# Kernel optimization log

Hardware: AMD Instinct MI355X
Metric: run time of the kernel (lower is better)

## Reference

```python
import jax, jax.numpy as jnp
import numpy as np

DIM = 128
HEADS = 4
DIM_HEAD = 32
EPS = 1e-5


def layer_norm(x, w, b):
    mu = jnp.mean(x, axis=-1, keepdims=True)
    var = jnp.mean(jnp.square(x - mu), axis=-1, keepdims=True)
    return (x - mu) * jax.lax.rsqrt(var + EPS) * w + b


def setup_inputs() -> dict:
    key = jax.random.key(0)
    ks = jax.random.split(key, 16)
    B, N, D, bH, bW = 2, 6, DIM, 50, 50
    iH, iW = 24, 56
    HD = HEADS * DIM_HEAD
    w = lambda k, shp: (jax.random.normal(k, shp, jnp.float32) * 0.02)
    inp = {
        "q": jax.random.normal(ks[0], (B, N, D, bH, bW), jnp.float32),
        "k": jax.random.normal(ks[1], (B, N, D, iH, iW), jnp.float32),
        "v": jax.random.normal(ks[2], (B, N, D, iH, iW), jnp.float32),
        "skip": jax.random.normal(ks[3], (B, D, bH, bW), jnp.float32),
        "ln_q_w": jnp.ones((D,), jnp.float32), "ln_q_b": jnp.zeros((D,), jnp.float32),
        "wq": w(ks[4], (D, HD)), "bq": jnp.zeros((HD,), jnp.float32),
        "ln_k_w": jnp.ones((D,), jnp.float32), "ln_k_b": jnp.zeros((D,), jnp.float32),
        "wk": w(ks[5], (D, HD)), "bk": jnp.zeros((HD,), jnp.float32),
        "ln_v_w": jnp.ones((D,), jnp.float32), "ln_v_b": jnp.zeros((D,), jnp.float32),
        "wv": w(ks[6], (D, HD)), "bv": jnp.zeros((HD,), jnp.float32),
        "wo": w(ks[7], (HD, D)), "bo": jnp.zeros((D,), jnp.float32),
        "ln_pre_w": jnp.ones((D,), jnp.float32), "ln_pre_b": jnp.zeros((D,), jnp.float32),
        "w1": w(ks[8], (D, 2 * D)), "b1": jnp.zeros((2 * D,), jnp.float32),
        "w2": w(ks[9], (2 * D, D)), "b2": jnp.zeros((D,), jnp.float32),
        "ln_post_w": jnp.ones((D,), jnp.float32), "ln_post_b": jnp.zeros((D,), jnp.float32),
    }
    return inp


def reference(q, k, v, skip,
              ln_q_w, ln_q_b, wq, bq,
              ln_k_w, ln_k_b, wk, bk,
              ln_v_w, ln_v_b, wv, bv,
              wo, bo, ln_pre_w, ln_pre_b,
              w1, b1, w2, b2, ln_post_w, ln_post_b):
    B, N, D, bH, bW = q.shape
    iH, iW = k.shape[-2:]
    Q, K = bH * bW, iH * iW
    scale = D ** (-0.5)  # NOTE: original uses dim**-0.5, not dim_head

    # queries: (B,N,D,Q) -> (B,N,Q,D) -> LN -> linear -> (B,N,Q,H,Dh)
    qf = jnp.transpose(q.reshape(B, N, D, Q), (0, 1, 3, 2))
    qh = (layer_norm(qf, ln_q_w, ln_q_b) @ wq + bq).reshape(B, N, Q, HEADS, DIM_HEAD)
    # keys: (B,N,D,K) -> (B,N,K,D)
    kf = jnp.transpose(k.reshape(B, N, D, K), (0, 1, 3, 2))
    kh = (layer_norm(kf, ln_k_w, ln_k_b) @ wk + bk).reshape(B, N, K, HEADS, DIM_HEAD)
    # values: (B,N,D,iH,iW) -> (B,N,iH,iW,D) -> (B,N*K,D)
    vf = jnp.transpose(v, (0, 1, 3, 4, 2)).reshape(B, N * K, D)
    vh = (layer_norm(vf, ln_v_w, ln_v_b) @ wv + bv).reshape(B, N * K, HEADS, DIM_HEAD)

    # logits: (B,N,Q,K,H) -> (B,Q,N*K,H), softmax over combined N*K axis
    logits = scale * jnp.einsum('bnqmd,bnkmd->bnqkm', qh, kh)
    logits = jnp.transpose(logits, (0, 2, 1, 3, 4)).reshape(B, Q, N * K, HEADS)
    att = jax.nn.softmax(logits, axis=-2)

    a = jnp.einsum('bqkm,bkmd->bqmd', att, vh).reshape(B, Q, HEADS * DIM_HEAD)
    z = a @ wo + bo  # (B,Q,D)
    z = z + jnp.transpose(skip.reshape(B, D, Q), (0, 2, 1))
    z = layer_norm(z, ln_pre_w, ln_pre_b)
    z = z + (jax.nn.gelu(z @ w1 + b1, approximate=False) @ w2 + b2)
    z = layer_norm(z, ln_post_w, ln_post_b)
    return jnp.transpose(z.reshape(B, bH, bW, D), (0, 3, 1, 2))
```

## Files before the change

kernel.cpp:

```cpp
#include <hip/hip_runtime.h>
#include <hip/hip_bf16.h>

#define QP 2500
#define KP 1344
#define SCALE 0.088388347648318447f
#define LOG2E 1.4426950408889634f
#define LNEPS 1e-5f

typedef __attribute__((ext_vector_type(8))) short bf16x8;
typedef __attribute__((ext_vector_type(4))) float f32x4;

__device__ inline ushort f2bf(float x) {
  uint u = __float_as_uint(x);
  return (ushort)((u + 0x7fffu + ((u >> 16) & 1u)) >> 16);
}

union Frag8 { uint2 u[2]; bf16x8 f; ushort us[8]; };

__device__ inline bf16x8 ldfrag_swz(const char* rowbase, int colbyte, int C) {
  Frag8 t;
  t.u[0] = *(const uint2*)(rowbase + ((colbyte) ^ C));
  t.u[1] = *(const uint2*)(rowbase + ((colbyte + 8) ^ C));
  return t.f;
}

__device__ inline uint pk2(float a, float b) {
  union { __hip_bfloat162 h; uint u; } cv;
  cv.h = __float22bfloat162_rn(make_float2(a, b));
  return cv.u;
}

__device__ inline void gld16(const ushort* g, ushort* l) {
  __builtin_amdgcn_global_load_lds(
      (const __attribute__((address_space(1))) void*)g,
      (__attribute__((address_space(3))) void*)l, 16, 0, 0);
}

__global__ __launch_bounds__(256) void wprep_kernel(
    const float* __restrict__ wq, const float* __restrict__ wk, const float* __restrict__ wv,
    ushort* __restrict__ wtq, ushort* __restrict__ wtk, ushort* __restrict__ wtv)
{
  const float* W = (blockIdx.y == 0) ? wq : (blockIdx.y == 1) ? wk : wv;
  ushort* WT = (blockIdx.y == 0) ? wtq : (blockIdx.y == 1) ? wtk : wtv;
  const int t = threadIdx.x;
  const int idx = blockIdx.x * 1024 + t * 4;
  const int k = idx >> 7, j0 = idx & 127;
  float4 rd = *(const float4*)&W[idx];
  WT[(j0 + 0) * 128 + k] = f2bf(rd.x);
  WT[(j0 + 1) * 128 + k] = f2bf(rd.y);
  WT[(j0 + 2) * 128 + k] = f2bf(rd.z);
  WT[(j0 + 3) * 128 + k] = f2bf(rd.w);
}

__global__ __launch_bounds__(256) void wprep2_kernel(
    const float* __restrict__ wo, const float* __restrict__ w1, const float* __restrict__ w2,
    ushort* __restrict__ woT, ushort* __restrict__ w1T, ushort* __restrict__ w2T)
{
  const int y = blockIdx.y;
  const float* W; ushort* WT; int jsh, K, total;
  if (y == 0)      { W = wo; WT = woT; jsh = 7; K = 128; total = 16384; }
  else if (y == 1) { W = w1; WT = w1T; jsh = 8; K = 128; total = 32768; }
  else             { W = w2; WT = w2T; jsh = 7; K = 256; total = 32768; }
  const int idx = blockIdx.x * 1024 + threadIdx.x * 4;
  if (idx >= total) return;
  const int k = idx >> jsh, j0 = idx & ((1 << jsh) - 1);
  float4 rd = *(const float4*)&W[idx];
  WT[(j0 + 0) * K + k] = f2bf(rd.x);
  WT[(j0 + 1) * K + k] = f2bf(rd.y);
  WT[(j0 + 2) * K + k] = f2bf(rd.z);
  WT[(j0 + 3) * K + k] = f2bf(rd.w);
}

__global__ __launch_bounds__(256) void proj_kernel(
    const float* __restrict__ qin, const float* __restrict__ kin, const float* __restrict__ vin,
    const float* __restrict__ lnqw, const float* __restrict__ lnqb,
    const float* __restrict__ lnkw, const float* __restrict__ lnkb,
    const float* __restrict__ lnvw, const float* __restrict__ lnvb,
    const ushort* __restrict__ wtq_, const ushort* __restrict__ wtk_, const ushort* __restrict__ wtv_,
    const float* __restrict__ bq_, const float* __restrict__ bk_, const float* __restrict__ bv_,
    ushort* __restrict__ qout, ushort* __restrict__ kout, ushort* __restrict__ vtout)
{
  const int z = blockIdx.z;
  if (z > 0 && blockIdx.x >= 21) return;

  const float *in, *lnw, *lnb, *bias;
  const ushort* WT;
  int P;
  if (z == 0)      { in = qin; lnw = lnqw; lnb = lnqb; WT = wtq_; bias = bq_; P = QP; }
  else if (z == 1) { in = kin; lnw = lnkw; lnb = lnkb; WT = wtk_; bias = bk_; P = KP; }
  else             { in = vin; lnw = lnvw; lnb = lnvb; WT = wtv_; bias = bv_; P = KP; }

  __shared__ __align__(16) ushort xb[64][128];
  __shared__ __align__(16) ushort wt[128][128];
  __shared__ float ps[4][64], pq[4][64];
  __shared__ float mu_s[64], rs_s[64];

  const int bn = blockIdx.y;
  const int p0 = blockIdx.x * 64;
  const int t  = threadIdx.x;
  const int w = t >> 6, lane = t & 63, g = lane >> 4, ln15 = lane & 15;

  #pragma unroll
  for (int i = 0; i < 8; ++i) {
    int idx8 = t + 256 * i;
    int j = idx8 >> 4, ck = (idx8 & 15) * 16;
    *(uint4*)((char*)wt + j * 256 + (ck ^ ((j & 7) << 4))) =
        *(const uint4*)((const char*)WT + j * 256 + ck);
  }

  const float* src = in + ((size_t)bn * 128) * P + p0;
  const int p = t & 63, dq = t >> 6;
  float xv[32];
  float s = 0.f, s2 = 0.f;
  #pragma unroll
  for (int kk = 0; kk < 32; ++kk) {
    int d = dq + 4 * kk;
    float v = (p0 + p < P) ? src[(size_t)d * P + p] : 0.f;
    xv[kk] = v; s += v; s2 += v * v;
  }
  ps[dq][p] = s; pq[dq][p] = s2;
  __syncthreads();
  if (t < 64) {
    float a = ps[0][t] + ps[1][t] + ps[2][t] + ps[3][t];
    float b = pq[0][t] + pq[1][t] + pq[2][t] + pq[3][t];
    float mu = a * (1.f / 128.f);
    float var = b * (1.f / 128.f) - mu * mu;
    mu_s[t] = mu; rs_s[t] = rsqrtf(var + LNEPS);
  }
  __syncthreads();
  {
    const float mu = mu_s[p], rs = rs_s[p];
    const int CW = (p & 7) << 4;
    #pragma unroll
    for (int kk = 0; kk < 32; ++kk) {
      int d = dq + 4 * kk;
      float v = (xv[kk] - mu) * rs * lnw[d] + lnb[d];
      *(ushort*)((char*)xb + p * 256 + ((2 * d) ^ CW)) = f2bf(v);
    }
  }
  __syncthreads();

  const int prow = w * 16 + ln15;
  const char* xrow = (const char*)xb + prow * 256;
  const int CX = (prow & 7) << 4;
  const int CB = (ln15 & 7) << 4;
  const f32x4 zf = {0.f, 0.f, 0.f, 0.f};
  f32x4 acc[8];
  #pragma unroll
  for (int jc = 0; jc < 8; ++jc) acc[jc] = zf;

  #pragma unroll
  for (int ks = 0; ks < 4; ++ks) {
    bf16x8 a = ldfrag_swz(xrow, ks * 64 + g * 16, CX);
    #pragma unroll
    for (int jc = 0; jc < 8; ++jc) {
      bf16x8 b = ldfrag_swz((const char*)wt + (jc * 16 + ln15) * 256, ks * 64 + g * 16, CB);
      acc[jc] = __builtin_amdgcn_mfma_f32_16x16x32_bf16(a, b, acc[jc], 0, 0, 0);
    }
  }

  if (z == 0) {
    const float os = SCALE * LOG2E;
    #pragma unroll
    for (int jc = 0; jc < 8; ++jc) {
      const float bj = bias[jc * 16 + ln15];
      #pragma unroll
      for (int r = 0; r < 4; ++r) {
        int pr = p0 + w * 16 + 4 * g + r;
        if (pr < P)
          qout[((size_t)bn * P + pr) * 128 + jc * 16 + ln15] = f2bf((acc[jc][r] + bj) * os);
      }
    }
  } else if (z == 1) {
    #pragma unroll
    for (int jc = 0; jc < 8; ++jc) {
      const int j = jc * 16 + ln15;
      const int h = j >> 5, dh = j & 31, gk = dh >> 3, pos = dh & 7;
      const float bj = bias[j];
      #pragma unroll
      for (int r4 = 0; r4 < 4; ++r4) {
        int pp = p0 + w * 16 + 4 * g + r4;
        int kt = pp >> 6, r = pp & 63;
        int ch = (gk + (r >> 1)) & 3;
        kout[(size_t)((bn * 4 + h) * 21 + kt) * 2048 + r * 32 + ch * 8 + pos] =
            f2bf(acc[jc][r4] + bj);
      }
    }
  } else {
    #pragma unroll
    for (int jc = 0; jc < 8; ++jc) {
      const int j = jc * 16 + ln15;
      const int h = j >> 5, rdh = j & 31;
      const float bj = bias[j];
      #pragma unroll
      for (int r4 = 0; r4 < 4; ++r4) {
        int pp = p0 + w * 16 + 4 * g + r4;
        int kt = pp >> 6, kk = pp & 63;
        int ch = (kk >> 3) ^ (rdh & 7);
        vtout[(size_t)((bn * 4 + h) * 21 + kt) * 2048 + rdh * 64 + ch * 8 + (kk & 7)] =
            f2bf(acc[jc][r4] + bj);
      }
    }
  }
}

__global__ __launch_bounds__(256, 4) void attn_kernel(
    const ushort* __restrict__ qh, const ushort* __restrict__ kimg,
    const ushort* __restrict__ vimg, float* __restrict__ aw,
    float* __restrict__ ml)
{
  __shared__ __align__(16) ushort Kb[2][2048];
  __shared__ __align__(16) ushort Vb[2][2048];
  __shared__ __align__(16) ushort Ps[4][32][64];

  const int lin = blockIdx.x + 20 * (blockIdx.y + 4 * blockIdx.z);
  const int sid = (lin & 7) * 120 + (lin >> 3);
  const int bx = sid % 20;
  const int hh = (sid / 20) & 3;
  const int bn = sid / 80;

  const int q0 = bx * 128;
  const int t = threadIdx.x;
  const int w = t >> 6, lane = t & 63;
  const int g = lane >> 4, ln15 = lane & 15;
  const int C = ((ln15 & 7) << 4) | (((ln15 >> 3) & 1) << 3);
  const int kch = (g + (ln15 >> 1)) & 3;
  const int vch0 = (0 + g) ^ (ln15 & 7);
  const int vch1 = (4 + g) ^ (ln15 & 7);

  bf16x8 qf0, qf1;
  {
    Frag8 z_; z_.u[0] = make_uint2(0, 0); z_.u[1] = make_uint2(0, 0);
    int qr0 = q0 + w * 32 + ln15;
    int qr1 = qr0 + 16;
    qf0 = (qr0 < QP) ? *(const bf16x8*)&qh[((size_t)bn * QP + qr0) * 128 + hh * 32 + g * 8] : z_.f;
    qf1 = (qr1 < QP) ? *(const bf16x8*)&qh[((size_t)bn * QP + qr1) * 128 + hh * 32 + g * 8] : z_.f;
  }

  Frag8 onesU;
  #pragma unroll
  for (int i = 0; i < 8; ++i) onesU.us[i] = 0x3F80;
  const bf16x8 ones = onesU.f;

  const ushort* ksrc = kimg + (size_t)((bn * 4 + hh) * 21) * 2048 + w * 512 + lane * 8;
  const ushort* vsrc = vimg + (size_t)((bn * 4 + hh) * 21) * 2048 + w * 512 + lane * 8;

  gld16(ksrc, &Kb[0][w * 512]);
  gld16(vsrc, &Vb[0][w * 512]);
  __syncthreads();

  const f32x4 zf = {0.f, 0.f, 0.f, 0.f};
  f32x4 o00 = zf, o01 = zf, o10 = zf, o11 = zf, ol0 = zf, ol1 = zf;

  for (int kt = 0; kt < 21; ++kt) {
    const int cur = kt & 1;
    if (kt < 20) {
      gld16(ksrc + (size_t)(kt + 1) * 2048, &Kb[cur ^ 1][w * 512]);
      gld16(vsrc + (size_t)(kt + 1) * 2048, &Vb[cur ^ 1][w * 512]);
    }

    const char* Kbase = (const char*)Kb[cur];
    const char* Vbase = (const char*)Vb[cur];
    char* Pw = (char*)Ps[w];

    f32x4 s0[4], s1[4];
    #pragma unroll
    for (int kb = 0; kb < 4; ++kb) {
      bf16x8 kf = *(const bf16x8*)(Kbase + (kb * 16 + ln15) * 64 + kch * 16);
      s0[kb] = __builtin_amdgcn_mfma_f32_16x16x32_bf16(kf, qf0, zf, 0, 0, 0);
      s1[kb] = __builtin_amdgcn_mfma_f32_16x16x32_bf16(kf, qf1, zf, 0, 0, 0);
    }

    {
      char* pr0 = Pw + ln15 * 128;
      char* pr1 = Pw + (16 + ln15) * 128;
      #pragma unroll
      for (int kb = 0; kb < 4; ++kb) {
        uint2 u;
        u.x = pk2(exp2f(s0[kb][0]), exp2f(s0[kb][1]));
        u.y = pk2(exp2f(s0[kb][2]), exp2f(s0[kb][3]));
        *(uint2*)(pr0 + ((kb * 32 + g * 8) ^ C)) = u;
        u.x = pk2(exp2f(s1[kb][0]), exp2f(s1[kb][1]));
        u.y = pk2(exp2f(s1[kb][2]), exp2f(s1[kb][3]));
        *(uint2*)(pr1 + ((kb * 32 + g * 8) ^ C)) = u;
      }
    }

    {
      const char* pr0 = Pw + ln15 * 128;
      const char* pr1 = Pw + (16 + ln15) * 128;
      #pragma unroll
      for (int kc = 0; kc < 2; ++kc) {
        bf16x8 pa0 = ldfrag_swz(pr0, kc * 64 + g * 16, C);
        bf16x8 pa1 = ldfrag_swz(pr1, kc * 64 + g * 16, C);
        const int vch = kc ? vch1 : vch0;
        bf16x8 vf0 = *(const bf16x8*)(Vbase + ln15 * 128 + vch * 16);
        bf16x8 vf1 = *(const bf16x8*)(Vbase + (16 + ln15) * 128 + vch * 16);
        o00 = __builtin_amdgcn_mfma_f32_16x16x32_bf16(pa0, vf0, o00, 0, 0, 0);
        o01 = __builtin_amdgcn_mfma_f32_16x16x32_bf16(pa0, vf1, o01, 0, 0, 0);
        o10 = __builtin_amdgcn_mfma_f32_16x16x32_bf16(pa1, vf0, o10, 0, 0, 0);
        o11 = __builtin_amdgcn_mfma_f32_16x16x32_bf16(pa1, vf1, o11, 0, 0, 0);
        ol0 = __builtin_amdgcn_mfma_f32_16x16x32_bf16(pa0, ones, ol0, 0, 0, 0);
        ol1 = __builtin_amdgcn_mfma_f32_16x16x32_bf16(pa1, ones, ol1, 0, 0, 0);
      }
    }
    __syncthreads();
  }

  if (ln15 == 0) {
    #pragma unroll
    for (int i = 0; i < 4; ++i) {
      int qr0 = q0 + w * 32 + 4 * g + i;
      int qr1 = qr0 + 16;
      if (qr0 < QP) ml[((size_t)bn * QP + qr0) * 4 + hh] = ol0[i];
      if (qr1 < QP) ml[((size_t)bn * QP + qr1) * 4 + hh] = ol1[i];
    }
  }
  #pragma unroll
  for (int i = 0; i < 4; ++i) {
    int qr0 = q0 + w * 32 + 4 * g + i;
    int qr1 = qr0 + 16;
    if (qr0 < QP) {
      size_t base = ((size_t)bn * QP + qr0) * 128 + hh * 32;
      aw[base + ln15] = o00[i];
      aw[base + 16 + ln15] = o01[i];
    }
    if (qr1 < QP) {
      size_t base = ((size_t)bn * QP + qr1) * 128 + hh * 32;
      aw[base + ln15] = o10[i];
      aw[base + 16 + ln15] = o11[i];
    }
  }
}

__global__ __launch_bounds__(256) void epilogue_kernel(
    const float* __restrict__ aw, const float* __restrict__ ml,
    const float* __restrict__ skip,
    const ushort* __restrict__ woT, const float* __restrict__ bo,
    const float* __restrict__ lnpw, const float* __restrict__ lnpb,
    const ushort* __restrict__ w1T, const float* __restrict__ b1,
    const ushort* __restrict__ w2T, const float* __restrict__ b2,
    const float* __restrict__ lnqw, const float* __restrict__ lnqb,
    float* __restrict__ out)
{
  __shared__ __align__(16) ushort xa[16][128];
  __shared__ __align__(16) ushort znb[16][128];
  __shared__ __align__(16) ushort hb[16][256];
  __shared__ float skp[128][17];
  __shared__ float2 red[4][16];
  __shared__ float mu_s[16], rs_s[16];
  __shared__ float cc[16][4];

  const int b = blockIdx.y;
  const int q0 = blockIdx.x * 16;
  const int t = threadIdx.x;
  const int w = t >> 6, lane = t & 63, g = lane >> 4, ln15 = lane & 15;
  const f32x4 zf = {0.f, 0.f, 0.f, 0.f};

  if (t < 64) {
    int r = t >> 2, h = t & 3;
    int qrow = q0 + r;
    float inv = 0.f;
    if (qrow < QP) {
      float sum = 0.f;
      #pragma unroll
      for (int n = 0; n < 6; ++n)
        sum += ml[((size_t)(b * 6 + n) * QP + qrow) * 4 + h];
      inv = 1.f / sum;
    }
    cc[r][h] = inv;
  }
  #pragma unroll
  for (int i = 0; i < 8; ++i) {
    int idx = t + 256 * i;
    int j = idx >> 4, r = idx & 15;
    int qrow = q0 + r;
    skp[j][r] = (qrow < QP) ? skip[((size_t)b * 128 + j) * QP + qrow] : 0.f;
  }
  __syncthreads();

  #pragma unroll
  for (int i = 0; i < 4; ++i) {
    int idx = t + 256 * i;
    int r = idx >> 6, jp = idx & 63;
    int qrow = q0 + r;
    float v0 = 0.f, v1 = 0.f;
    if (qrow < QP) {
      #pragma unroll
      for (int n = 0; n < 6; ++n) {
        float2 p = *(const float2*)&aw[((size_t)(b * 6 + n) * QP + qrow) * 128 + 2 * jp];
        v0 += p.x; v1 += p.y;
      }
      float iv = cc[r][jp >> 4];
      v0 *= iv; v1 *= iv;
    }
    *(uint*)((char*)xa + r * 256 + ((4 * jp) ^ ((r & 7) << 4))) = pk2(v0, v1);
  }
  __syncthreads();

  f32x4 acc1[2] = {zf, zf};
  #pragma unroll
  for (int ks = 0; ks < 4; ++ks) {
    bf16x8 a = ldfrag_swz((const char*)xa + ln15 * 256, ks * 64 + g * 16, (ln15 & 7) << 4);
    #pragma unroll
    for (int jc = 0; jc < 2; ++jc) {
      int j = (2 * w + jc) * 16 + ln15;
      bf16x8 bfr = *(const bf16x8*)&woT[j * 128 + ks * 32 + g * 8];
      acc1[jc] = __builtin_amdgcn_mfma_f32_16x16x32_bf16(a, bfr, acc1[jc], 0, 0, 0);
    }
  }
  float z[2][4];
  #pragma unroll
  for (int jc = 0; jc < 2; ++jc) {
    int j = (2 * w + jc) * 16 + ln15;
    float bj = bo[j];
    #pragma unroll
    for (int i = 0; i < 4; ++i)
      z[jc][i] = acc1[jc][i] + bj + skp[j][4 * g + i];
  }
  {
    float s_[4], q_[4];
    #pragma unroll
    for (int i = 0; i < 4; ++i) {
      s_[i] = z[0][i] + z[1][i];
      q_[i] = z[0][i] * z[0][i] + z[1][i] * z[1][i];
    }
    #pragma unroll
    for (int m = 1; m <= 8; m <<= 1) {
      #pragma unroll
      for (int i = 0; i < 4; ++i) {
        s_[i] += __shfl_xor(s_[i], m);
        q_[i] += __shfl_xor(q_[i], m);
      }
    }
    if (ln15 == 0) {
      #pragma unroll
      for (int i = 0; i < 4; ++i) red[w][4 * g + i] = make_float2(s_[i], q_[i]);
    }
  }
  __syncthreads();
  if (t < 16) {
    float S = red[0][t].x + red[1][t].x + red[2][t].x + red[3][t].x;
    float Q = red[0][t].y + red[1][t].y + red[2][t].y + red[3][t].y;
    float mu = S * (1.f / 128.f);
    float var = Q * (1.f / 128.f) - mu * mu;
    mu_s[t] = mu; rs_s[t] = rsqrtf(var + LNEPS);
  }
  __syncthreads();
  float zn[2][4];
  #pragma unroll
  for (int jc = 0; jc < 2; ++jc) {
    int j = (2 * w + jc) * 16 + ln15;
    float lw = lnpw[j], lb = lnpb[j];
    #pragma unroll
    for (int i = 0; i < 4; ++i) {
      int r = 4 * g + i;
      float v = (z[jc][i] - mu_s[r]) * rs_s[r] * lw + lb;
      zn[jc][i] = v;
      *(ushort*)((char*)znb + r * 256 + ((2 * j) ^ ((r & 7) << 4))) = f2bf(v);
    }
  }
  __syncthreads();

  f32x4 acc2[4] = {zf, zf, zf, zf};
  #pragma unroll
  for (int ks = 0; ks < 4; ++ks) {
    bf16x8 a = ldfrag_swz((const char*)znb + ln15 * 256, ks * 64 + g * 16, (ln15 & 7) << 4);
    #pragma unroll
    for (int jc2 = 0; jc2 < 4; ++jc2) {
      int j2 = (4 * w + jc2) * 16 + ln15;
      bf16x8 bfr = *(const bf16x8*)&w1T[j2 * 128 + ks * 32 + g * 8];
      acc2[jc2] = __builtin_amdgcn_mfma_f32_16x16x32_bf16(a, bfr, acc2[jc2], 0, 0, 0);
    }
  }
  #pragma unroll
  for (int jc2 = 0; jc2 < 4; ++jc2) {
    int j2 = (4 * w + jc2) * 16 + ln15;
    float bj = b1[j2];
    #pragma unroll
    for (int i = 0; i < 4; ++i) {
      float x = acc2[jc2][i] + bj;
      float ge = 0.5f * x * (1.f + erff(x * 0.70710678118654752f));
      int r = 4 * g + i;
      *(ushort*)((char*)hb + r * 512 + ((2 * j2) ^ ((r & 7) << 4))) = f2bf(ge);
    }
  }
  __syncthreads();

  f32x4 acc3[2] = {zf, zf};
  #pragma unroll
  for (int ks = 0; ks < 8; ++ks) {
    bf16x8 a = ldfrag_swz((const char*)hb + ln15 * 512, ks * 64 + g * 16, (ln15 & 7) << 4);
    #pragma unroll
    for (int jc = 0; jc < 2; ++jc) {
      int j = (2 * w + jc) * 16 + ln15;
      bf16x8 bfr = *(const bf16x8*)&w2T[j * 256 + ks * 32 + g * 8];
      acc3[jc] = __builtin_amdgcn_mfma_f32_16x16x32_bf16(a, bfr, acc3[jc], 0, 0, 0);
    }
  }
  float z2[2][4];
  #pragma unroll
  for (int jc = 0; jc < 2; ++jc) {
    int j = (2 * w + jc) * 16 + ln15;
    float bj = b2[j];
    #pragma unroll
    for (int i = 0; i < 4; ++i)
      z2[jc][i] = acc3[jc][i] + bj + zn[jc][i];
  }
  {
    float s_[4], q_[4];
    #pragma unroll
    for (int i = 0; i < 4; ++i) {
      s_[i] = z2[0][i] + z2[1][i];
      q_[i] = z2[0][i] * z2[0][i] + z2[1][i] * z2[1][i];
    }
    #pragma unroll
    for (int m = 1; m <= 8; m <<= 1) {
      #pragma unroll
      for (int i = 0; i < 4; ++i) {
        s_[i] += __shfl_xor(s_[i], m);
        q_[i] += __shfl_xor(q_[i], m);
      }
    }
    if (ln15 == 0) {
      #pragma unroll
      for (int i = 0; i < 4; ++i) red[w][4 * g + i] = make_float2(s_[i], q_[i]);
    }
  }
  __syncthreads();
  if (t < 16) {
    float S = red[0][t].x + red[1][t].x + red[2][t].x + red[3][t].x;
    float Q = red[0][t].y + red[1][t].y + red[2][t].y + red[3][t].y;
    float mu = S * (1.f / 128.f);
    float var = Q * (1.f / 128.f) - mu * mu;
    mu_s[t] = mu; rs_s[t] = rsqrtf(var + LNEPS);
  }
  __syncthreads();
  #pragma unroll
  for (int jc = 0; jc < 2; ++jc) {
    int j = (2 * w + jc) * 16 + ln15;
    float lw = lnqw[j], lb = lnqb[j];
    #pragma unroll
    for (int i = 0; i < 4; ++i) {
      int r = 4 * g + i;
      skp[j][r] = (z2[jc][i] - mu_s[r]) * rs_s[r] * lw + lb;
    }
  }
  __syncthreads();
  #pragma unroll
  for (int i = 0; i < 8; ++i) {
    int idx = t + 256 * i;
    int j = idx >> 4, r = idx & 15;
    int qrow = q0 + r;
    if (qrow < QP)
      out[((size_t)b * 128 + j) * QP + qrow] = skp[j][r];
  }
}

extern "C" void kernel_launch(void* const* d_in, const int* in_sizes, int n_in,
                              void* d_out, int out_size, void* d_ws, size_t ws_size,
                              hipStream_t stream) {
  const float* q       = (const float*)d_in[0];
  const float* k       = (const float*)d_in[1];
  const float* v       = (const float*)d_in[2];
  const float* skip    = (const float*)d_in[3];
  const float* ln_q_w  = (const float*)d_in[4];
  const float* ln_q_b  = (const float*)d_in[5];
  const float* wq      = (const float*)d_in[6];
  const float* bq      = (const float*)d_in[7];
  const float* ln_k_w  = (const float*)d_in[8];
  const float* ln_k_b  = (const float*)d_in[9];
  const float* wk      = (const float*)d_in[10];
  const float* bk      = (const float*)d_in[11];
  const float* ln_v_w  = (const float*)d_in[12];
  const float* ln_v_b  = (const float*)d_in[13];
  const float* wv      = (const float*)d_in[14];
  const float* bv      = (const float*)d_in[15];
  const float* wo      = (const float*)d_in[16];
  const float* bo      = (const float*)d_in[17];
  const float* ln_pre_w  = (const float*)d_in[18];
  const float* ln_pre_b  = (const float*)d_in[19];
  const float* w1      = (const float*)d_in[20];
  const float* b1      = (const float*)d_in[21];
  const float* w2      = (const float*)d_in[22];
  const float* b2      = (const float*)d_in[23];
  const float* ln_post_w = (const float*)d_in[24];
  const float* ln_post_b = (const float*)d_in[25];

  float* out = (float*)d_out;
  ushort* qhp  = (ushort*)d_ws;
  ushort* kimg = qhp + 3840000;
  ushort* vimg = kimg + 2064384;
  ushort* wtq  = vimg + 2064384;
  ushort* wtk  = wtq + 16384;
  ushort* wtv  = wtk + 16384;
  ushort* woT  = wtv + 16384;
  ushort* w1T  = woT + 16384;
  ushort* w2T  = w1T + 32768;
  float*  aw   = (float*)(w2T + 32768);
  float*  ml   = aw + 3840000;

  wprep_kernel<<<dim3(16, 3), 256, 0, stream>>>(wq, wk, wv, wtq, wtk, wtv);
  wprep2_kernel<<<dim3(32, 3), 256, 0, stream>>>(wo, w1, w2, woT, w1T, w2T);
  proj_kernel<<<dim3(40, 12, 3), 256, 0, stream>>>(q, k, v,
      ln_q_w, ln_q_b, ln_k_w, ln_k_b, ln_v_w, ln_v_b,
      wtq, wtk, wtv, bq, bk, bv, qhp, kimg, vimg);
  attn_kernel<<<dim3(20, 4, 12), 256, 0, stream>>>(qhp, kimg, vimg, aw, ml);
  epilogue_kernel<<<dim3(157, 2), 256, 0, stream>>>(aw, ml, skip, woT, bo,
      ln_pre_w, ln_pre_b, w1T, b1, w2T, b2, ln_post_w, ln_post_b, out);
}
```

Baseline: 112.4 us.

## Load K/V fragments directly from global in attention, merge weight-prep kernels

Result: faster. 109.7 us (-2.5%).

```diff
diff --git a/kernel.cpp b/kernel.cpp
--- a/kernel.cpp
+++ b/kernel.cpp
@@ -30,37 +30,22 @@
   return cv.u;
 }
 
-__device__ inline void gld16(const ushort* g, ushort* l) {
-  __builtin_amdgcn_global_load_lds(
-      (const __attribute__((address_space(1))) void*)g,
-      (__attribute__((address_space(3))) void*)l, 16, 0, 0);
-}
-
 __global__ __launch_bounds__(256) void wprep_kernel(
     const float* __restrict__ wq, const float* __restrict__ wk, const float* __restrict__ wv,
-    ushort* __restrict__ wtq, ushort* __restrict__ wtk, ushort* __restrict__ wtv)
-{
-  const float* W = (blockIdx.y == 0) ? wq : (blockIdx.y == 1) ? wk : wv;
-  ushort* WT = (blockIdx.y == 0) ? wtq : (blockIdx.y == 1) ? wtk : wtv;
-  const int t = threadIdx.x;
-  const int idx = blockIdx.x * 1024 + t * 4;
-  const int k = idx >> 7, j0 = idx & 127;
-  float4 rd = *(const float4*)&W[idx];
-  WT[(j0 + 0) * 128 + k] = f2bf(rd.x);
-  WT[(j0 + 1) * 128 + k] = f2bf(rd.y);
-  WT[(j0 + 2) * 128 + k] = f2bf(rd.z);
-  WT[(j0 + 3) * 128 + k] = f2bf(rd.w);
-}
-
-__global__ __launch_bounds__(256) void wprep2_kernel(
     const float* __restrict__ wo, const float* __restrict__ w1, const float* __restrict__ w2,
+    ushort* __restrict__ wtq, ushort* __restrict__ wtk, ushort* __restrict__ wtv,
     ushort* __restrict__ woT, ushort* __restrict__ w1T, ushort* __restrict__ w2T)
 {
   const int y = blockIdx.y;
   const float* W; ushort* WT; int jsh, K, total;
-  if (y == 0)      { W = wo; WT = woT; jsh = 7; K = 128; total = 16384; }
-  else if (y == 1) { W = w1; WT = w1T; jsh = 8; K = 128; total = 32768; }
-  else             { W = w2; WT = w2T; jsh = 7; K = 256; total = 32768; }
+  switch (y) {
+    case 0: W = wq; WT = wtq; jsh = 7; K = 128; total = 16384; break;
+    case 1: W = wk; WT = wtk; jsh = 7; K = 128; total = 16384; break;
+    case 2: W = wv; WT = wtv; jsh = 7; K = 128; total = 16384; break;
+    case 3: W = wo; WT = woT; jsh = 7; K = 128; total = 16384; break;
+    case 4: W = w1; WT = w1T; jsh = 8; K = 128; total = 32768; break;
+    default: W = w2; WT = w2T; jsh = 7; K = 256; total = 32768; break;
+  }
   const int idx = blockIdx.x * 1024 + threadIdx.x * 4;
   if (idx >= total) return;
   const int k = idx >> jsh, j0 = idx & ((1 << jsh) - 1);
@@ -209,8 +194,6 @@
     const ushort* __restrict__ vimg, float* __restrict__ aw,
     float* __restrict__ ml)
 {
-  __shared__ __align__(16) ushort Kb[2][2048];
-  __shared__ __align__(16) ushort Vb[2][2048];
   __shared__ __align__(16) ushort Ps[4][32][64];
 
   const int lin = blockIdx.x + 20 * (blockIdx.y + 4 * blockIdx.z);
@@ -242,34 +225,27 @@
   for (int i = 0; i < 8; ++i) onesU.us[i] = 0x3F80;
   const bf16x8 ones = onesU.f;
 
-  const ushort* ksrc = kimg + (size_t)((bn * 4 + hh) * 21) * 2048 + w * 512 + lane * 8;
-  const ushort* vsrc = vimg + (size_t)((bn * 4 + hh) * 21) * 2048 + w * 512 + lane * 8;
-
-  gld16(ksrc, &Kb[0][w * 512]);
-  gld16(vsrc, &Vb[0][w * 512]);
-  __syncthreads();
+  const size_t slab = (size_t)((bn * 4 + hh) * 21) * 2048;
+  const ushort* kfp = kimg + slab + ln15 * 32 + kch * 8;
+  const ushort* vb0 = vimg + slab + ln15 * 64;
+  const ushort* vb1 = vb0 + 16 * 64;
 
   const f32x4 zf = {0.f, 0.f, 0.f, 0.f};
   f32x4 o00 = zf, o01 = zf, o10 = zf, o11 = zf, ol0 = zf, ol1 = zf;
 
   for (int kt = 0; kt < 21; ++kt) {
-    const int cur = kt & 1;
-    if (kt < 20) {
-      gld16(ksrc + (size_t)(kt + 1) * 2048, &Kb[cur ^ 1][w * 512]);
-      gld16(vsrc + (size_t)(kt + 1) * 2048, &Vb[cur ^ 1][w * 512]);
-    }
-
-    const char* Kbase = (const char*)Kb[cur];
-    const char* Vbase = (const char*)Vb[cur];
+    const ushort* kp = kfp + (size_t)kt * 2048;
     char* Pw = (char*)Ps[w];
 
     f32x4 s0[4], s1[4];
+    __builtin_amdgcn_s_setprio(1);
     #pragma unroll
     for (int kb = 0; kb < 4; ++kb) {
-      bf16x8 kf = *(const bf16x8*)(Kbase + (kb * 16 + ln15) * 64 + kch * 16);
+      bf16x8 kf = *(const bf16x8*)(kp + kb * 512);
       s0[kb] = __builtin_amdgcn_mfma_f32_16x16x32_bf16(kf, qf0, zf, 0, 0, 0);
       s1[kb] = __builtin_amdgcn_mfma_f32_16x16x32_bf16(kf, qf1, zf, 0, 0, 0);
     }
+    __builtin_amdgcn_s_setprio(0);
 
     {
       char* pr0 = Pw + ln15 * 128;
@@ -287,24 +263,27 @@
     }
 
     {
-      const char* pr0 = Pw + ln15 * 128;
-      const char* pr1 = Pw + (16 + ln15) * 128;
+      const char* pr0 = (const char*)Ps[w] + ln15 * 128;
+      const char* pr1 = (const char*)Ps[w] + (16 + ln15) * 128;
+      const ushort* vt0 = vb0 + (size_t)kt * 2048;
+      const ushort* vt1 = vb1 + (size_t)kt * 2048;
       #pragma unroll
       for (int kc = 0; kc < 2; ++kc) {
         bf16x8 pa0 = ldfrag_swz(pr0, kc * 64 + g * 16, C);
         bf16x8 pa1 = ldfrag_swz(pr1, kc * 64 + g * 16, C);
         const int vch = kc ? vch1 : vch0;
-        bf16x8 vf0 = *(const bf16x8*)(Vbase + ln15 * 128 + vch * 16);
-        bf16x8 vf1 = *(const bf16x8*)(Vbase + (16 + ln15) * 128 + vch * 16);
+        bf16x8 vf0 = *(const bf16x8*)(vt0 + vch * 8);
+        bf16x8 vf1 = *(const bf16x8*)(vt1 + vch * 8);
+        __builtin_amdgcn_s_setprio(1);
         o00 = __builtin_amdgcn_mfma_f32_16x16x32_bf16(pa0, vf0, o00, 0, 0, 0);
         o01 = __builtin_amdgcn_mfma_f32_16x16x32_bf16(pa0, vf1, o01, 0, 0, 0);
         o10 = __builtin_amdgcn_mfma_f32_16x16x32_bf16(pa1, vf0, o10, 0, 0, 0);
         o11 = __builtin_amdgcn_mfma_f32_16x16x32_bf16(pa1, vf1, o11, 0, 0, 0);
         ol0 = __builtin_amdgcn_mfma_f32_16x16x32_bf16(pa0, ones, ol0, 0, 0, 0);
         ol1 = __builtin_amdgcn_mfma_f32_16x16x32_bf16(pa1, ones, ol1, 0, 0, 0);
-      }
-    }
-    __syncthreads();
+        __builtin_amdgcn_s_setprio(0);
+      }
+    }
   }
 
   if (ln15 == 0) {
@@ -600,8 +579,8 @@
   float*  aw   = (float*)(w2T + 32768);
   float*  ml   = aw + 3840000;
 
-  wprep_kernel<<<dim3(16, 3), 256, 0, stream>>>(wq, wk, wv, wtq, wtk, wtv);
-  wprep2_kernel<<<dim3(32, 3), 256, 0, stream>>>(wo, w1, w2, woT, w1T, w2T);
+  wprep_kernel<<<dim3(32, 6), 256, 0, stream>>>(wq, wk, wv, wo, w1, w2,
+      wtq, wtk, wtv, woT, w1T, w2T);
   proj_kernel<<<dim3(40, 12, 3), 256, 0, stream>>>(q, k, v,
       ln_q_w, ln_q_b, ln_k_w, ln_k_b, ln_v_w, ln_v_b,
       wtq, wtk, wtv, bq, bk, bv, qhp, kimg, vimg);
```
